# Performance work log

Measured on AMD Instinct MI355X. Metric: run time of the kernel, lower is better.

## Reference

```python
import jax, jax.numpy as jnp
import numpy as np

LN_EPS = 1e-5
EPSILON = 1e-8
NUM_ITERS = 3
SLOT_SIZE = 128
NUM_SLOTS = 7
MLP_HIDDEN = 256


def _layernorm(x, g, b):
    m = jnp.mean(x, axis=-1, keepdims=True)
    v = jnp.var(x, axis=-1, keepdims=True)
    return (x - m) * jax.lax.rsqrt(v + LN_EPS) * g + b


def setup_inputs() -> dict:
    key = jax.random.key(0)
    ks = jax.random.split(key, 16)
    B, N, D, S, H, M = 64, 4096, 128, NUM_SLOTS, SLOT_SIZE, MLP_HIDDEN
    sc = 0.05
    return {
        "inputs": jax.random.normal(ks[0], (B, N, D), jnp.float32),
        "slots_init": jax.random.normal(ks[1], (B, S, H + 4), jnp.float32),
        "ln_in_g": jnp.ones((D,), jnp.float32), "ln_in_b": jnp.zeros((D,), jnp.float32),
        "ln_s_g": jnp.ones((H,), jnp.float32), "ln_s_b": jnp.zeros((H,), jnp.float32),
        "ln_m_g": jnp.ones((H,), jnp.float32), "ln_m_b": jnp.zeros((H,), jnp.float32),
        "Wq": jax.random.normal(ks[2], (H, H), jnp.float32) * sc,
        "Wk": jax.random.normal(ks[3], (H, H), jnp.float32) * sc,
        "Wv": jax.random.normal(ks[4], (H, H), jnp.float32) * sc,
        "W_ih": jax.random.normal(ks[5], (3 * H, H), jnp.float32) * sc,
        "W_hh": jax.random.normal(ks[6], (3 * H, H), jnp.float32) * sc,
        "b_ih": jnp.zeros((3 * H,), jnp.float32),
        "b_hh": jnp.zeros((3 * H,), jnp.float32),
        "mlp_w1": jax.random.normal(ks[7], (M, H), jnp.float32) * sc,
        "mlp_b1": jnp.zeros((M,), jnp.float32),
        "mlp_w2": jax.random.normal(ks[8], (H, M), jnp.float32) * sc,
        "mlp_b2": jnp.zeros((H,), jnp.float32),
        "slots_mu": jax.random.normal(ks[9], (1, 1, H + 4), jnp.float32) * sc,
        "slots_log_sigma": jax.random.normal(ks[10], (1, 1, H + 4), jnp.float32) * sc,
    }


def _gru_cell(x, h, W_ih, W_hh, b_ih, b_hh):
    # torch.nn.GRUCell math; x, h: [..., H]
    gi = x @ W_ih.T + b_ih
    gh = h @ W_hh.T + b_hh
    i_r, i_z, i_n = jnp.split(gi, 3, axis=-1)
    h_r, h_z, h_n = jnp.split(gh, 3, axis=-1)
    r = jax.nn.sigmoid(i_r + h_r)
    z = jax.nn.sigmoid(i_z + h_z)
    n = jnp.tanh(i_n + r * h_n)
    return (1.0 - z) * n + z * h


def reference(inputs, slots_init, ln_in_g, ln_in_b, ln_s_g, ln_s_b, ln_m_g, ln_m_b,
              Wq, Wk, Wv, W_ih, W_hh, b_ih, b_hh, mlp_w1, mlp_b1, mlp_w2, mlp_b2,
              slots_mu, slots_log_sigma):
    x = _layernorm(inputs, ln_in_g, ln_in_b)           # [B, N, D]
    k = x @ Wk.T                                       # [B, N, H]
    v = x @ Wv.T                                       # [B, N, H]
    slots_full = slots_mu + jnp.exp(slots_log_sigma) * slots_init  # [B, S, H+4]
    slots = slots_full[..., :SLOT_SIZE]                # positions/scales discarded
    scale = SLOT_SIZE ** -0.5
    for _ in range(NUM_ITERS):
        slots_prev = slots
        sn = _layernorm(slots, ln_s_g, ln_s_b)
        q = sn @ Wq.T                                  # [B, S, H]
        logits = scale * jnp.einsum('bnh,bsh->bns', k, q)
        attn = jax.nn.softmax(logits, axis=-1) + EPSILON
        attn = attn / jnp.sum(attn, axis=1, keepdims=True)
        updates = jnp.einsum('bns,bnh->bsh', attn, v)  # [B, S, H]
        slots = _gru_cell(updates, slots_prev, W_ih, W_hh, b_ih, b_hh)
        slots = slots + (jax.nn.relu(_layernorm(slots, ln_m_g, ln_m_b) @ mlp_w1.T + mlp_b1) @ mlp_w2.T + mlp_b2)
    return slots
```

## Files before the change

kernel.cpp:

```cpp
#include <hip/hip_runtime.h>
#include <hip/hip_bf16.h>
#include <stdint.h>

typedef unsigned int u32;
typedef unsigned short u16;
typedef float v2f __attribute__((ext_vector_type(2)));
typedef short bf16x8 __attribute__((ext_vector_type(8)));
typedef float f32x4 __attribute__((ext_vector_type(4)));

#define LN_EPS_ 1e-5f
#define EPS_ 1e-8f

__device__ __forceinline__ float bflo(u32 v){ return __uint_as_float(v << 16); }
__device__ __forceinline__ float bfhi(u32 v){ return __uint_as_float(v & 0xFFFF0000u); }
__device__ __forceinline__ u32 f2bf(float f){
    u32 x = __float_as_uint(f);
    return (x + 0x7FFFu + ((x >> 16) & 1u)) >> 16;
}
__device__ __forceinline__ u32 pack2bf(float a, float b){
    union { __hip_bfloat162 h; u32 u; } cv;
    cv.h = __float22bfloat162_rn(float2{a, b});
    return cv.u;
}
__device__ __forceinline__ v2f pkfma(v2f a, v2f b, v2f c){
    v2f d; asm("v_pk_fma_f32 %0, %1, %2, %3" : "=v"(d) : "v"(a), "v"(b), "v"(c)); return d;
}
__device__ __forceinline__ v2f pkadd(v2f a, v2f b){
    v2f d; asm("v_pk_add_f32 %0, %1, %2" : "=v"(d) : "v"(a), "v"(b)); return d;
}
__device__ __forceinline__ bf16x8 as_bf16x8(uint4 u){
    union { uint4 a; bf16x8 b; } c; c.a = u; return c.b;
}

__global__ __launch_bounds__(256) void k_pack(
    const float* __restrict__ Wq, const float* __restrict__ Wv,
    const float* __restrict__ Wih, const float* __restrict__ Whh,
    const float* __restrict__ w1, const float* __restrict__ w2,
    float* __restrict__ WqT, u32* __restrict__ Pv, u32* __restrict__ Pih,
    u32* __restrict__ Phh, u32* __restrict__ Pw1, u32* __restrict__ Pw2,
    u32* __restrict__ Rg32)
{
    int i = blockIdx.x * 256 + threadIdx.x;
    if (i < 8192) {
        int dp = i >> 7, o = i & 127;
        Pv[i] = pack2bf(Wv[o * 128 + 2 * dp], Wv[o * 128 + 2 * dp + 1]);
    } else if (i < 32768) {
        int r = i - 8192; int dp = r / 384, j = r - dp * 384;
        Pih[r] = pack2bf(Wih[j * 128 + 2 * dp], Wih[j * 128 + 2 * dp + 1]);
    } else if (i < 57344) {
        int r = i - 32768; int dp = r / 384, j = r - dp * 384;
        Phh[r] = pack2bf(Whh[j * 128 + 2 * dp], Whh[j * 128 + 2 * dp + 1]);
    } else if (i < 73728) {
        int r = i - 57344; int dp = r >> 8, j = r & 255;
        Pw1[r] = pack2bf(w1[j * 128 + 2 * dp], w1[j * 128 + 2 * dp + 1]);
    } else if (i < 90112) {
        int r = i - 73728; int mp = r >> 7, o = r & 127;
        Pw2[r] = pack2bf(w2[o * 256 + 2 * mp], w2[o * 256 + 2 * mp + 1]);
    } else if (i < 106496) {
        int r = i - 90112; int d = r >> 7, o = r & 127;
        WqT[r] = Wq[o * 128 + d];
    } else if (i < 143360) {
        int r = i - 106496; int b = r / 576, rem = r - b * 576;
        Rg32[b * 1024 + 448 + rem] = 0;
    }
}

__global__ __launch_bounds__(256) void k_init_prep(
    const float* __restrict__ slots_init, const float* __restrict__ mu,
    const float* __restrict__ ls, float* __restrict__ slots,
    const float* __restrict__ g_s, const float* __restrict__ b_s,
    const float* __restrict__ WqT, const float* __restrict__ Wk,
    const float* __restrict__ g_in, const float* __restrict__ b_in,
    u16* __restrict__ Rg, float* __restrict__ c1ws, float* __restrict__ c2ws)
{
    __shared__ float snb[128], qb[128], xch[128], red4[4];
    int bs = blockIdx.x, t = threadIdx.x;
    int b = bs / 7, s = bs - b * 7;
    int h = t & 127, half = t >> 7;
    float nv = 0.f;
    if (!half) {
        nv = mu[h] + expf(ls[h]) * slots_init[bs * 132 + h];
        slots[bs * 128 + h] = nv;
    }
    if (!half) {
        float smv = nv, sqv = nv * nv;
        for (int m = 32; m >= 1; m >>= 1) { smv += __shfl_xor(smv, m); sqv += __shfl_xor(sqv, m); }
        if ((t & 63) == 0) { red4[(t >> 6) * 2] = smv; red4[(t >> 6) * 2 + 1] = sqv; }
    }
    __syncthreads();
    float mean = (red4[0] + red4[2]) * (1.0f / 128.0f);
    float var  = (red4[1] + red4[3]) * (1.0f / 128.0f) - mean * mean;
    float rsv = rsqrtf(var + LN_EPS_);
    if (!half) snb[h] = (nv - mean) * rsv * g_s[h] + b_s[h];
    __syncthreads();
    {
        float q0 = 0.f, q1 = 0.f;
        int d0 = half * 64;
        #pragma unroll 4
        for (int d = d0; d < d0 + 64; d += 2) {
            q0 += WqT[d * 128 + h] * snb[d];
            q1 += WqT[(d + 1) * 128 + h] * snb[d + 1];
        }
        if (half) xch[h] = q0 + q1;
        __syncthreads();
        if (!half) qb[h] = q0 + q1 + xch[h];
        __syncthreads();
    }
    float r0 = 0.f, r1 = 0.f;
    int j0 = half * 64;
    #pragma unroll 4
    for (int j = j0; j < j0 + 64; j += 2) {
        r0 += Wk[j * 128 + h] * qb[j];
        r1 += Wk[(j + 1) * 128 + h] * qb[j + 1];
    }
    if (half) xch[h] = r0 + r1;
    __syncthreads();
    if (!half) {
        float r = (r0 + r1 + xch[h]) * 0.08838834764831845f;
        float rt  = g_in[h] * r;
        float c2v = b_in[h] * r;
        Rg[((size_t)b * 16 + s) * 128 + h] = (u16)f2bf(rt);
        float c1p = rt, c2p = c2v;
        for (int m = 32; m >= 1; m >>= 1) { c1p += __shfl_xor(c1p, m); c2p += __shfl_xor(c2p, m); }
        if ((t & 63) == 0) { red4[(t >> 6) * 2] = c1p; red4[(t >> 6) * 2 + 1] = c2p; }
    }
    __syncthreads();
    if (t == 0) {
        c1ws[b * 8 + s] = red4[0] + red4[2];
        c2ws[b * 8 + s] = red4[1] + red4[3];
    }
}

__global__ __launch_bounds__(256, 8) void k_attn(
    const float* __restrict__ xin,
    const u16* __restrict__ Rg, const float* __restrict__ c1ws,
    const float* __restrict__ c2ws,
    float* __restrict__ ypart, float* __restrict__ Zp, float* __restrict__ Ap,
    u32* __restrict__ Xbf, float* __restrict__ Sg, int first)
{
    __shared__ u32 tile[4096];
    __shared__ __align__(16) float wt[448];
    __shared__ __align__(8)  float stats[128];
    __shared__ float c1l[16], c2l[16];
    __shared__ float redp[4][8], redw[4][8];
    int t = threadIdx.x;
    int b = blockIdx.y;
    int n0 = blockIdx.x * 64;
    int lane = t & 63, wv = t >> 6;
    int ls = lane & 15, lg = lane >> 4;
    size_t blk = (size_t)b * 64 + blockIdx.x;

    if (t < 16) {
        c1l[t] = (t < 7) ? c1ws[b * 8 + t] : 0.f;
        c2l[t] = (t < 7) ? c2ws[b * 8 + t] : 0.f;
    }

    bf16x8 bfr[4];
    {
        const u16* Rrow = Rg + ((size_t)b * 16 + ls) * 128;
        #pragma unroll
        for (int kk = 0; kk < 4; kk++)
            bfr[kk] = as_bf16x8(*(const uint4*)&Rrow[kk * 32 + lg * 8]);
    }

    if (first) {
        int r = t >> 2, p = t & 3;
        const float4* xg = (const float4*)(xin + ((size_t)b * 4096 + n0 + r) * 128 + p * 32);
        v2f smp = (v2f){0.f, 0.f}, sqp = (v2f){0.f, 0.f};
        #pragma unroll
        for (int i = 0; i < 8; i++) {
            float4 v = xg[i];
            v2f lo = (v2f){v.x, v.y}, hi = (v2f){v.z, v.w};
            smp = pkadd(smp, pkadd(lo, hi));
            sqp = pkfma(lo, lo, sqp);
            sqp = pkfma(hi, hi, sqp);
            int q = p * 4 + (i >> 1), rem = (i & 1) * 2;
            *(uint2*)&tile[(r * 16 + (q ^ (r & 15))) * 4 + rem] =
                make_uint2(pack2bf(v.x, v.y), pack2bf(v.z, v.w));
        }
        float sm = smp.x + smp.y, sq = sqp.x + sqp.y;
        sm += __shfl_xor(sm, 1); sq += __shfl_xor(sq, 1);
        sm += __shfl_xor(sm, 2); sq += __shfl_xor(sq, 2);
        if (!p) {
            float mean = sm * (1.0f / 128.0f);
            float var  = sq * (1.0f / 128.0f) - mean * mean;
            *(float2*)&stats[2 * r] = make_float2(mean, rsqrtf(var + LN_EPS_));
        }
        __syncthreads();
        uint4* dst = (uint4*)(Xbf + blk * 4096);
        const uint4* srcT = (const uint4*)tile;
        #pragma unroll
        for (int j = 0; j < 4; j++) dst[j * 256 + t] = srcT[j * 256 + t];
        if (t < 128) Sg[blk * 128 + t] = stats[t];
    } else {
        uint4* dstT = (uint4*)tile;
        const uint4* src = (const uint4*)(Xbf + blk * 4096);
        #pragma unroll
        for (int j = 0; j < 4; j++) dstT[j * 256 + t] = src[j * 256 + t];
        if (t < 128) stats[t] = Sg[blk * 128 + t];
        __syncthreads();
    }

    f32x4 acc0 = {0.f, 0.f, 0.f, 0.f};
    {
        int m0 = wv * 16 + ls;
        #pragma unroll
        for (int kk = 0; kk < 4; kk++) {
            int q = kk * 4 + lg;
            bf16x8 a0 = as_bf16x8(*(const uint4*)&tile[(m0 * 16 + (q ^ ls)) * 4]);
            acc0 = __builtin_amdgcn_mfma_f32_16x16x32_bf16(a0, bfr[kk], acc0, 0, 0, 0);
        }
    }
    {
        float zsum = 0.f, asum = 0.f;
        float c1v = c1l[ls], c2v = c2l[ls];
        bool sv = ls < 7;
        int nbase = wv * 16 + lg * 4;
        #pragma unroll
        for (int r4 = 0; r4 < 4; r4++) {
            int n = nbase + r4;
            float2 stf = *(const float2*)&stats[2 * n];
            float L = sv ? (stf.y * (acc0[r4] - stf.x * c1v) + c2v) : -3.4e38f;
            float mx = L;
            mx = fmaxf(mx, __shfl_xor(mx, 1));
            mx = fmaxf(mx, __shfl_xor(mx, 2));
            mx = fmaxf(mx, __shfl_xor(mx, 4));
            mx = fmaxf(mx, __shfl_xor(mx, 8));
            float e = __expf(L - mx);
            float ssum = e;
            ssum += __shfl_xor(ssum, 1);
            ssum += __shfl_xor(ssum, 2);
            ssum += __shfl_xor(ssum, 4);
            ssum += __shfl_xor(ssum, 8);
            float p = e * (1.0f / ssum) + EPS_;
            float w = p * stf.y;
            if (sv) {
                wt[ls * 64 + n] = w;
                zsum += p;
                asum += w * stf.x;
            }
        }
        zsum += __shfl_xor(zsum, 16); zsum += __shfl_xor(zsum, 32);
        asum += __shfl_xor(asum, 16); asum += __shfl_xor(asum, 32);
        if (lane < 7) { redp[wv][lane] = zsum; redw[wv][lane] = asum; }
    }
    __syncthreads();
    if (t < 7)
        Zp[blk * 8 + t] = redp[0][t] + redp[1][t] + redp[2][t] + redp[3][t];
    else if (t >= 64 && t < 71) {
        int s = t - 64;
        Ap[blk * 8 + s] = redw[0][s] + redw[1][s] + redw[2][s] + redw[3][s];
    }

    int nh = t >> 7, dp = t & 63, sA = (t >> 6) & 1;
    v2f aclo[4], achi[4];
    #pragma unroll
    for (int k = 0; k < 4; k++) { aclo[k] = (v2f){0.f,0.f}; achi[k] = (v2f){0.f,0.f}; }
    int nbeg = nh * 32;
    #pragma unroll 4
    for (int n = nbeg; n < nbeg + 32; n += 2) {
        u32 x0 = tile[(n * 16 + ((dp >> 2) ^ (n & 15))) * 4 + (dp & 3)];
        u32 x1 = tile[((n + 1) * 16 + ((dp >> 2) ^ ((n + 1) & 15))) * 4 + (dp & 3)];
        v2f alo = (v2f){bflo(x0), bflo(x1)};
        v2f ahi = (v2f){bfhi(x0), bfhi(x1)};
        #pragma unroll
        for (int k = 0; k < 4; k++) {
            int s = sA + 2 * k;
            if (s < 7) {
                v2f wp = *(const v2f*)&wt[s * 64 + n];
                aclo[k] = pkfma(alo, wp, aclo[k]);
                achi[k] = pkfma(ahi, wp, achi[k]);
            }
        }
    }
    float* yp = ypart + (blk * 2 + nh) * 896;
    #pragma unroll
    for (int k = 0; k < 4; k++) {
        int s = sA + 2 * k;
        if (s < 7) {
            *(float2*)&yp[s * 128 + 2 * dp] =
                make_float2(aclo[k].x + aclo[k].y, achi[k].x + achi[k].y);
        }
    }
}

__global__ __launch_bounds__(512) void k_update(
    float* __restrict__ slots, const float* __restrict__ ypart,
    const float* __restrict__ Zp, const float* __restrict__ Ap,
    const float* __restrict__ g_in, const float* __restrict__ b_in,
    const u32* __restrict__ Pv, const u32* __restrict__ Pih,
    const u32* __restrict__ Phh, const float* __restrict__ b_ih,
    const float* __restrict__ b_hh, const float* __restrict__ g_m,
    const float* __restrict__ b_m, const u32* __restrict__ Pw1,
    const float* __restrict__ bb1, const u32* __restrict__ Pw2,
    const float* __restrict__ bb2, float* __restrict__ out,
    const float* __restrict__ g_s, const float* __restrict__ b_s,
    const float* __restrict__ WqT, const float* __restrict__ Wk,
    u16* __restrict__ Rg, float* __restrict__ c1ws, float* __restrict__ c2ws,
    int do_prep)
{
    __shared__ float ybuf[128], ub[128], hb[128], lb[128], t1b[256];
    __shared__ float red4w[4][128];
    __shared__ float g6[12][128];
    __shared__ float m1p[256];
    __shared__ float redA[2], redB[2];
    __shared__ float snb[128], qb[128], red4[4];
    __shared__ float Zsh, Ash;
    int bs = blockIdx.x, t = threadIdx.x;
    int b = bs / 7, s = bs - b * 7;
    int h = t & 127, q = t >> 7;
    {
        float ysum = 0.f;
        const float* bp = ypart + ((size_t)(b * 128 + q * 32)) * 896 + s * 128 + h;
        #pragma unroll 8
        for (int c = 0; c < 32; c++) ysum += bp[(size_t)c * 896];
        red4w[q][h] = ysum;
    }
    if (t < 64) {
        float z = Zp[((size_t)b * 64 + t) * 8 + s];
        for (int m = 32; m >= 1; m >>= 1) z += __shfl_xor(z, m);
        if (t == 0) Zsh = z;
    } else if (t < 128) {
        float a_ = Ap[((size_t)b * 64 + (t - 64)) * 8 + s];
        for (int m = 32; m >= 1; m >>= 1) a_ += __shfl_xor(a_, m);
        if (t == 64) Ash = a_;
    }
    __syncthreads();
    if (q == 0) {
        float ytot = red4w[0][h] + red4w[1][h] + red4w[2][h] + red4w[3][h];
        ybuf[h] = g_in[h] * (ytot - Ash) / Zsh + b_in[h];
        hb[h] = slots[bs * 128 + h];
    }
    __syncthreads();
    {
        float a0 = 0.f;
        int dp0 = q * 16;
        #pragma unroll 4
        for (int dp = dp0; dp < dp0 + 16; dp++) {
            u32 w0 = Pv[dp * 128 + h];
            a0 += bflo(w0) * ybuf[2 * dp] + bfhi(w0) * ybuf[2 * dp + 1];
        }
        red4w[q][h] = a0;
    }
    __syncthreads();
    if (q == 0) ub[h] = red4w[0][h] + red4w[1][h] + red4w[2][h] + red4w[3][h];
    __syncthreads();
    {
        const u32* P = (q >= 2) ? Phh : Pih;
        const float* src = (q >= 2) ? hb : ub;
        int dp0 = (q & 1) * 32;
        float gv0 = 0.f, gv1 = 0.f, gv2 = 0.f;
        #pragma unroll 4
        for (int dp = dp0; dp < dp0 + 32; dp++) {
            float x0 = src[2 * dp], x1 = src[2 * dp + 1];
            u32 w0 = P[dp * 384 + h];
            u32 w1v = P[dp * 384 + 128 + h];
            u32 w2v = P[dp * 384 + 256 + h];
            gv0 += bflo(w0) * x0 + bfhi(w0) * x1;
            gv1 += bflo(w1v) * x0 + bfhi(w1v) * x1;
            gv2 += bflo(w2v) * x0 + bfhi(w2v) * x1;
        }
        g6[q * 3 + 0][h] = gv0; g6[q * 3 + 1][h] = gv1; g6[q * 3 + 2][h] = gv2;
    }
    __syncthreads();
    float hv = 0.f;
    if (q == 0) {
        float gi0 = g6[0][h] + g6[3][h] + b_ih[h];
        float gi1 = g6[1][h] + g6[4][h] + b_ih[128 + h];
        float gi2 = g6[2][h] + g6[5][h] + b_ih[256 + h];
        float gh0 = g6[6][h] + g6[9][h]  + b_hh[h];
        float gh1 = g6[7][h] + g6[10][h] + b_hh[128 + h];
        float gh2 = g6[8][h] + g6[11][h] + b_hh[256 + h];
        float rg = 1.0f / (1.0f + __expf(-(gi0 + gh0)));
        float zg = 1.0f / (1.0f + __expf(-(gi1 + gh1)));
        float ng = tanhf(gi2 + rg * gh2);
        hv = (1.0f - zg) * ng + zg * hb[h];
        float sm2 = hv, sq2 = hv * hv;
        for (int m = 32; m >= 1; m >>= 1) { sm2 += __shfl_xor(sm2, m); sq2 += __shfl_xor(sq2, m); }
        if ((t & 63) == 0) { redA[t >> 6] = sm2; redB[t >> 6] = sq2; }
    }
    __syncthreads();
    if (q == 0) {
        float sm2 = redA[0] + redA[1], sq2 = redB[0] + redB[1];
        float mean = sm2 * (1.0f / 128.0f);
        float var  = sq2 * (1.0f / 128.0f) - mean * mean;
        float rsq = rsqrtf(var + LN_EPS_);
        lb[h] = (hv - mean) * rsq * g_m[h] + b_m[h];
    }
    __syncthreads();
    {
        int o = t & 255, kh = t >> 8;
        float m1 = 0.f;
        int dp0 = kh * 32;
        #pragma unroll 4
        for (int dp = dp0; dp < dp0 + 32; dp++) {
            u32 w0 = Pw1[dp * 256 + o];
            m1 += bflo(w0) * lb[2 * dp] + bfhi(w0) * lb[2 * dp + 1];
        }
        if (kh) m1p[o] = m1;
        __syncthreads();
        if (!kh) t1b[o] = fmaxf(m1 + m1p[o] + bb1[o], 0.0f);
    }
    __syncthreads();
    {
        float o0 = 0.f;
        int mp0 = q * 32;
        #pragma unroll 4
        for (int mp = mp0; mp < mp0 + 32; mp++) {
            u32 w0 = Pw2[mp * 128 + h];
            o0 += bflo(w0) * t1b[2 * mp] + bfhi(w0) * t1b[2 * mp + 1];
        }
        red4w[q][h] = o0;
    }
    __syncthreads();
    float nv = 0.f;
    if (q == 0) {
        nv = hv + bb2[h] + red4w[0][h] + red4w[1][h] + red4w[2][h] + red4w[3][h];
        slots[bs * 128 + h] = nv;
        out[bs * 128 + h] = nv;
    }
    if (do_prep) {
        __syncthreads();
        if (q == 0) {
            float smv = nv, sqv = nv * nv;
            for (int m = 32; m >= 1; m >>= 1) { smv += __shfl_xor(smv, m); sqv += __shfl_xor(sqv, m); }
            if ((t & 63) == 0) { red4[(t >> 6) * 2] = smv; red4[(t >> 6) * 2 + 1] = sqv; }
        }
        __syncthreads();
        float mean = (red4[0] + red4[2]) * (1.0f / 128.0f);
        float var  = (red4[1] + red4[3]) * (1.0f / 128.0f) - mean * mean;
        float rsv = rsqrtf(var + LN_EPS_);
        if (q == 0) snb[h] = (nv - mean) * rsv * g_s[h] + b_s[h];
        __syncthreads();
        {
            float qv = 0.f;
            int d0 = q * 32;
            #pragma unroll 4
            for (int d = d0; d < d0 + 32; d++) qv += WqT[d * 128 + h] * snb[d];
            red4w[q][h] = qv;
        }
        __syncthreads();
        if (q == 0) qb[h] = red4w[0][h] + red4w[1][h] + red4w[2][h] + red4w[3][h];
        __syncthreads();
        {
            float rv = 0.f;
            int j0 = q * 32;
            #pragma unroll 4
            for (int j = j0; j < j0 + 32; j++) rv += Wk[j * 128 + h] * qb[j];
            red4w[q][h] = rv;
        }
        __syncthreads();
        if (q == 0) {
            float r = (red4w[0][h] + red4w[1][h] + red4w[2][h] + red4w[3][h])
                      * 0.08838834764831845f;
            float rt  = g_in[h] * r;
            float c2v = b_in[h] * r;
            Rg[((size_t)b * 16 + s) * 128 + h] = (u16)f2bf(rt);
            float c1p = rt, c2p = c2v;
            for (int m = 32; m >= 1; m >>= 1) { c1p += __shfl_xor(c1p, m); c2p += __shfl_xor(c2p, m); }
            if ((t & 63) == 0) { red4[(t >> 6) * 2] = c1p; red4[(t >> 6) * 2 + 1] = c2p; }
        }
        __syncthreads();
        if (t == 0) {
            c1ws[b * 8 + s] = red4[0] + red4[2];
            c2ws[b * 8 + s] = red4[1] + red4[3];
        }
    }
}

extern "C" void kernel_launch(void* const* d_in, const int* in_sizes, int n_in,
                              void* d_out, int out_size, void* d_ws, size_t ws_size,
                              hipStream_t stream) {
    const float* inputs     = (const float*)d_in[0];
    const float* slots_init = (const float*)d_in[1];
    const float* ln_in_g    = (const float*)d_in[2];
    const float* ln_in_b    = (const float*)d_in[3];
    const float* ln_s_g     = (const float*)d_in[4];
    const float* ln_s_b     = (const float*)d_in[5];
    const float* ln_m_g     = (const float*)d_in[6];
    const float* ln_m_b     = (const float*)d_in[7];
    const float* Wq         = (const float*)d_in[8];
    const float* Wk         = (const float*)d_in[9];
    const float* Wv         = (const float*)d_in[10];
    const float* W_ih       = (const float*)d_in[11];
    const float* W_hh       = (const float*)d_in[12];
    const float* b_ih       = (const float*)d_in[13];
    const float* b_hh       = (const float*)d_in[14];
    const float* mlp_w1     = (const float*)d_in[15];
    const float* mlp_b1     = (const float*)d_in[16];
    const float* mlp_w2     = (const float*)d_in[17];
    const float* mlp_b2     = (const float*)d_in[18];
    const float* slots_mu   = (const float*)d_in[19];
    const float* slots_ls   = (const float*)d_in[20];

    char* ws = (char*)d_ws;
    float* slots = (float*)(ws);
    u16*   Rg    = (u16*)  (ws + 229376);
    float* c1ws  = (float*)(ws + 491520);
    float* c2ws  = (float*)(ws + 493568);
    float* WqT   = (float*)(ws + 495616);
    u32*   Pv    = (u32*)  (ws + 561152);
    u32*   Pih   = (u32*)  (ws + 593920);
    u32*   Phh   = (u32*)  (ws + 692224);
    u32*   Pw1   = (u32*)  (ws + 790528);
    u32*   Pw2   = (u32*)  (ws + 856064);
    float* Zp    = (float*)(ws + 921600);
    float* Ap    = (float*)(ws + 1052672);
    float* ypart = (float*)(ws + 1183744);
    u32*   Xbf   = (u32*)  (ws + 30543872);
    float* Sg    = (float*)(ws + 97652736);

    k_pack<<<560, 256, 0, stream>>>(Wq, Wv, W_ih, W_hh, mlp_w1, mlp_w2,
                                    WqT, Pv, Pih, Phh, Pw1, Pw2, (u32*)Rg);
    k_init_prep<<<448, 256, 0, stream>>>(slots_init, slots_mu, slots_ls, slots,
                                         ln_s_g, ln_s_b, WqT, Wk, ln_in_g, ln_in_b,
                                         Rg, c1ws, c2ws);
    for (int it = 0; it < 3; it++) {
        k_attn<<<dim3(64, 64), 256, 0, stream>>>(inputs, Rg, c1ws, c2ws,
                                                 ypart, Zp, Ap,
                                                 Xbf, Sg, (it == 0) ? 1 : 0);
        k_update<<<448, 512, 0, stream>>>(slots, ypart, Zp, Ap, ln_in_g, ln_in_b,
                                          Pv, Pih, Phh, b_ih, b_hh,
                                          ln_m_g, ln_m_b, Pw1, mlp_b1, Pw2, mlp_b2,
                                          (float*)d_out,
                                          ln_s_g, ln_s_b, WqT, Wk,
                                          Rg, c1ws, c2ws, (it < 2) ? 1 : 0);
    }
}
```

Before: 402.6 us.

## Drop bf16 input cache and reduce attention partials in-block before global write

Removes the cached bf16 copy of the normalized inputs, so each iteration re-reads the fp32 inputs and recomputes row stats instead of writing and re-reading a bf16 workspace. The two per-block halves of the update partial sums are combined through shared memory, halving the ypart writes and the reads in the update kernel. This trades extra input-read bandwidth in later iterations for less workspace traffic and simpler control flow.

```diff
diff --git a/kernel.cpp b/kernel.cpp
--- a/kernel.cpp
+++ b/kernel.cpp
@@ -135,8 +135,7 @@
     const float* __restrict__ xin,
     const u16* __restrict__ Rg, const float* __restrict__ c1ws,
     const float* __restrict__ c2ws,
-    float* __restrict__ ypart, float* __restrict__ Zp, float* __restrict__ Ap,
-    u32* __restrict__ Xbf, float* __restrict__ Sg, int first)
+    float* __restrict__ ypart, float* __restrict__ Zp, float* __restrict__ Ap)
 {
     __shared__ u32 tile[4096];
     __shared__ __align__(16) float wt[448];
@@ -163,7 +162,7 @@
             bfr[kk] = as_bf16x8(*(const uint4*)&Rrow[kk * 32 + lg * 8]);
     }
 
-    if (first) {
+    {
         int r = t >> 2, p = t & 3;
         const float4* xg = (const float4*)(xin + ((size_t)b * 4096 + n0 + r) * 128 + p * 32);
         v2f smp = (v2f){0.f, 0.f}, sqp = (v2f){0.f, 0.f};
@@ -186,20 +185,8 @@
             float var  = sq * (1.0f / 128.0f) - mean * mean;
             *(float2*)&stats[2 * r] = make_float2(mean, rsqrtf(var + LN_EPS_));
         }
-        __syncthreads();
-        uint4* dst = (uint4*)(Xbf + blk * 4096);
-        const uint4* srcT = (const uint4*)tile;
-        #pragma unroll
-        for (int j = 0; j < 4; j++) dst[j * 256 + t] = srcT[j * 256 + t];
-        if (t < 128) Sg[blk * 128 + t] = stats[t];
-    } else {
-        uint4* dstT = (uint4*)tile;
-        const uint4* src = (const uint4*)(Xbf + blk * 4096);
-        #pragma unroll
-        for (int j = 0; j < 4; j++) dstT[j * 256 + t] = src[j * 256 + t];
-        if (t < 128) stats[t] = Sg[blk * 128 + t];
-        __syncthreads();
-    }
+    }
+    __syncthreads();
 
     f32x4 acc0 = {0.f, 0.f, 0.f, 0.f};
     {
@@ -273,13 +260,29 @@
             }
         }
     }
-    float* yp = ypart + (blk * 2 + nh) * 896;
-    #pragma unroll
-    for (int k = 0; k < 4; k++) {
-        int s = sA + 2 * k;
-        if (s < 7) {
-            *(float2*)&yp[s * 128 + 2 * dp] =
-                make_float2(aclo[k].x + aclo[k].y, achi[k].x + achi[k].y);
+    float* ytmp = (float*)tile;
+    __syncthreads();
+    if (nh) {
+        #pragma unroll
+        for (int k = 0; k < 4; k++) {
+            int s = sA + 2 * k;
+            if (s < 7)
+                *(float2*)&ytmp[s * 128 + 2 * dp] =
+                    make_float2(aclo[k].x + aclo[k].y, achi[k].x + achi[k].y);
+        }
+    }
+    __syncthreads();
+    if (!nh) {
+        float* yp = ypart + blk * 896;
+        #pragma unroll
+        for (int k = 0; k < 4; k++) {
+            int s = sA + 2 * k;
+            if (s < 7) {
+                float2 o = *(const float2*)&ytmp[s * 128 + 2 * dp];
+                *(float2*)&yp[s * 128 + 2 * dp] =
+                    make_float2(aclo[k].x + aclo[k].y + o.x,
+                                achi[k].x + achi[k].y + o.y);
+            }
         }
     }
 }
@@ -311,9 +314,9 @@
     int h = t & 127, q = t >> 7;
     {
         float ysum = 0.f;
-        const float* bp = ypart + ((size_t)(b * 128 + q * 32)) * 896 + s * 128 + h;
+        const float* bp = ypart + ((size_t)(b * 64 + q * 16)) * 896 + s * 128 + h;
         #pragma unroll 8
-        for (int c = 0; c < 32; c++) ysum += bp[(size_t)c * 896];
+        for (int c = 0; c < 16; c++) ysum += bp[(size_t)c * 896];
         red4w[q][h] = ysum;
     }
     if (t < 64) {
@@ -507,8 +510,6 @@
     float* Zp    = (float*)(ws + 921600);
     float* Ap    = (float*)(ws + 1052672);
     float* ypart = (float*)(ws + 1183744);
-    u32*   Xbf   = (u32*)  (ws + 30543872);
-    float* Sg    = (float*)(ws + 97652736);
 
     k_pack<<<560, 256, 0, stream>>>(Wq, Wv, W_ih, W_hh, mlp_w1, mlp_w2,
                                     WqT, Pv, Pih, Phh, Pw1, Pw2, (u32*)Rg);
@@ -517,8 +518,7 @@
                                          Rg, c1ws, c2ws);
     for (int it = 0; it < 3; it++) {
         k_attn<<<dim3(64, 64), 256, 0, stream>>>(inputs, Rg, c1ws, c2ws,
-                                                 ypart, Zp, Ap,
-                                                 Xbf, Sg, (it == 0) ? 1 : 0);
+                                                 ypart, Zp, Ap);
         k_update<<<448, 512, 0, stream>>>(slots, ypart, Zp, Ap, ln_in_g, ln_in_b,
                                           Pv, Pih, Phh, b_ih, b_hh,
                                           ln_m_g, ln_m_b, Pw1, mlp_b1, Pw2, mlp_b2,
```

Measured after the change: 368.8 us. -8.4%, faster.
